# Optimization experiments

Measured on AMD Instinct MI355X. Metric: run time of the kernel, lower is better.

Reference implementation:

```python
import jax, jax.numpy as jnp
import numpy as np
from jax import lax

B, N, T, F, H, R = 32, 1024, 32, 5, 64, 5


def setup_inputs() -> dict:
    key = jax.random.key(0)
    ks = jax.random.split(key, 12)
    sc = 0.1
    x = jax.random.normal(ks[0], (B, N, T, F), dtype=jnp.float32)
    A = jax.random.randint(ks[1], (N, N, R), 0, 2).astype(jnp.float32)
    return {
        "x": x,
        "A": A,
        # nn.LSTM params (torch layout: [4H, in], gate order i,f,g,o)
        "lstm_Wih": jax.random.normal(ks[2], (4 * H, F), dtype=jnp.float32) * sc,
        "lstm_Whh": jax.random.normal(ks[3], (4 * H, H), dtype=jnp.float32) * sc,
        "lstm_bih": jax.random.normal(ks[4], (4 * H,), dtype=jnp.float32) * sc,
        "lstm_bhh": jax.random.normal(ks[5], (4 * H,), dtype=jnp.float32) * sc,
        # attention Linear(H, 1)
        "attn_w": jax.random.normal(ks[6], (1, H), dtype=jnp.float32) * sc,
        "attn_b": jax.random.normal(ks[7], (1,), dtype=jnp.float32) * sc,
        # GNN edge-gate Linear(R, 1)
        "gnn_w": jax.random.normal(ks[8], (1, R), dtype=jnp.float32) * sc,
        "gnn_b": jax.random.normal(ks[9], (1,), dtype=jnp.float32) * sc,
        # pred Linear(2H, 1)
        "pred_w": jax.random.normal(ks[10], (1, 2 * H), dtype=jnp.float32) * sc,
        "pred_b": jax.random.normal(ks[11], (1,), dtype=jnp.float32) * sc,
    }


def _lstm_attn(x, Wih, Whh, bih, bhh, attn_w, attn_b):
    # x: [BN, T, F] -> attended hidden [BN, H]
    BN, Tt, _ = x.shape
    Hh = Whh.shape[1]
    pre = x @ Wih.T + (bih + bhh)  # [BN, T, 4H] input projections precomputed

    def step(carry, xt):
        h, c = carry
        gates = xt + h @ Whh.T
        i, f, g, o = jnp.split(gates, 4, axis=-1)
        c = jax.nn.sigmoid(f) * c + jax.nn.sigmoid(i) * jnp.tanh(g)
        h = jax.nn.sigmoid(o) * jnp.tanh(c)
        return (h, c), h

    init = (jnp.zeros((BN, Hh), x.dtype), jnp.zeros((BN, Hh), x.dtype))
    _, hs = lax.scan(step, init, pre.transpose(1, 0, 2))
    hs = hs.transpose(1, 0, 2)  # [BN, T, H]
    scores = jnp.tanh(hs @ attn_w.T + attn_b)      # [BN, T, 1]
    aw = jax.nn.softmax(scores, axis=1)            # softmax over time
    return jnp.sum(hs * aw, axis=1)                # [BN, H]


def reference(x, A, lstm_Wih, lstm_Whh, lstm_bih, lstm_bhh,
              attn_w, attn_b, gnn_w, gnn_b, pred_w, pred_b):
    Bb, Nn, Tt, Ff = x.shape
    Hh = lstm_Whh.shape[1]
    # LSTM+attention shared across stocks -> fold stocks into batch
    e_old = _lstm_attn(x.reshape(Bb * Nn, Tt, Ff), lstm_Wih, lstm_Whh,
                       lstm_bih, lstm_bhh, attn_w, attn_b).reshape(Bb, Nn, Hh)

    # GNN: per-edge gate w[i,j] = LeakyReLU(Linear(A[i,j,:])), active if sum(A[i,j])>0
    mask = (jnp.sum(A, axis=-1) > 0).astype(e_old.dtype)             # [N, N]
    w = jax.nn.leaky_relu((A @ gnn_w.T + gnn_b)[..., 0], 0.2)        # [N, N]
    deg = jnp.sum(mask, axis=1)                                      # [N] active neighbor count
    coef = mask * w                                                  # [N, N]
    dots = jnp.einsum('bik,bjk->bij', e_old, e_old)                  # [B, N, N]
    e_new = jnp.einsum('bij,ij,bjk->bik', dots, coef, e_old) / deg[None, :, None]
    e_final = jnp.concatenate([e_old, e_new], axis=-1)               # [B, N, 2H]
    preds = e_final @ pred_w.T + pred_b                              # [B, N, 1]
    return preds
```

## Files before the change

kernel.cpp:

```cpp
#include <hip/hip_runtime.h>

constexpr int Bc = 32, Nc = 1024, Tc = 32, Fc = 5, Hc = 64;
constexpr int BNc = Bc * Nc;

#define DEVFN __device__ __forceinline__

typedef _Float16 f16x8 __attribute__((ext_vector_type(8)));
typedef _Float16 f16x4 __attribute__((ext_vector_type(4)));
typedef float    f32x16 __attribute__((ext_vector_type(16)));

DEVFN float fast_rcp(float x) { return __builtin_amdgcn_rcpf(x); }
DEVFN float tanh_fast(float x) { return 1.f - 2.f * fast_rcp(__expf(2.f * x) + 1.f); }

__global__ __launch_bounds__(128, 2) void lstm_attn_kernel(
    const float* __restrict__ x,
    const float* __restrict__ Wih,
    const float* __restrict__ Whh,
    const float* __restrict__ bih,
    const float* __restrict__ bhh,
    const float* __restrict__ attn_w,
    const float* __restrict__ attn_b,
    _Float16* __restrict__ E16,
    _Float16* __restrict__ ET)
{
    constexpr int XP = 164;
    __shared__ __align__(16) _Float16 xs[32 * XP];
    __shared__ __align__(16) _Float16 hb[2][32 * 64];
    __shared__ float ap[2][32];
    float* es = (float*)xs;

    const int tid  = threadIdx.x;
    const int w    = tid >> 6;
    const int lane = tid & 63;
    const int m    = lane & 31;
    const int hi   = lane >> 5;

    const float* xg = x + (size_t)blockIdx.x * 32 * Tc * Fc;
    for (int i = tid; i < 32 * 160; i += 128) {
        int mm = i / 160, o = i - mm * 160;
        xs[mm * XP + o] = (_Float16)xg[i];
    }
    for (int i = tid; i < 1024; i += 128) ((uint*)&hb[0][0])[i] = 0u;

    f16x8 af[4][5];
    #pragma unroll
    for (int g = 0; g < 4; ++g) {
        const int j = 32 * (2 * g + w) + m;
        #pragma unroll
        for (int kt = 0; kt < 4; ++kt) {
            const float* wp = Whh + j * 64 + kt * 16 + 8 * hi;
            float4 u0 = *(const float4*)wp;
            float4 u1 = *(const float4*)(wp + 4);
            af[g][kt] = f16x8{(_Float16)u0.x, (_Float16)u0.y, (_Float16)u0.z, (_Float16)u0.w,
                              (_Float16)u1.x, (_Float16)u1.y, (_Float16)u1.z, (_Float16)u1.w};
        }
        float v[8];
        #pragma unroll
        for (int e = 0; e < 5; ++e) v[e] = Wih[j * Fc + e];
        v[5] = bih[j] + bhh[j]; v[6] = 0.f; v[7] = 0.f;
        #pragma unroll
        for (int e = 0; e < 8; ++e) {
            float z = hi ? 0.f : v[e];
            af[g][4][e] = (_Float16)z;
        }
    }

    float aw_own[16];
    #pragma unroll
    for (int a2 = 0; a2 < 4; ++a2)
        #pragma unroll
        for (int p = 0; p < 4; ++p)
            aw_own[a2 * 4 + p] = attn_w[32 * w + 8 * a2 + 4 * hi + p];
    const float ab = attn_b[0];

    float hcur[16], cst[16], oacc[16];
    #pragma unroll
    for (int i = 0; i < 16; ++i) { hcur[i] = 0.f; cst[i] = 0.f; oacc[i] = 0.f; }
    float lsum = 0.f;

    f32x16 zero16 = {0,0,0,0,0,0,0,0,0,0,0,0,0,0,0,0};
    const int xrow = m * XP;
    const int swz  = m & 15;
    __syncthreads();

    f16x8 bf[5];
    #pragma unroll
    for (int kt = 0; kt < 4; ++kt) {
        f16x4 lo = *(const f16x4*)&hb[0][m * 64 + ((4 * kt + 2 * hi)     ^ swz) * 4];
        f16x4 hh = *(const f16x4*)&hb[0][m * 64 + ((4 * kt + 2 * hi + 1) ^ swz) * 4];
        bf[kt] = f16x8{lo[0], lo[1], lo[2], lo[3], hh[0], hh[1], hh[2], hh[3]};
    }
    {
        #pragma unroll
        for (int e = 0; e < 8; ++e) bf[4][e] = (_Float16)0.f;
        if (!hi) {
            #pragma unroll
            for (int e = 0; e < 5; ++e) bf[4][e] = xs[xrow + e];
            bf[4][5] = (_Float16)1.f;
        }
    }

    #pragma unroll 1
    for (int t = 0; t < Tc; ++t) {
        f32x16 acc[4];
        #pragma unroll
        for (int g = 0; g < 4; ++g) {
            acc[g] = __builtin_amdgcn_mfma_f32_32x32x16_f16(af[g][0], bf[0], zero16, 0, 0, 0);
            #pragma unroll
            for (int kt = 1; kt < 5; ++kt)
                acc[g] = __builtin_amdgcn_mfma_f32_32x32x16_f16(af[g][kt], bf[kt], acc[g], 0, 0, 0);
        }
        float attnp = 0.f;
        #pragma unroll
        for (int r = 0; r < 16; ++r) {
            float ei = __expf(-acc[0][r]);
            float ef = __expf(-acc[1][r]);
            float Eg = __expf(2.f * acc[2][r]);
            float eo = __expf(-acc[3][r]);
            float u  = 1.f + ei;
            float v  = 1.f + ef;
            float wq = Eg + 1.f;
            float z  = Eg - 1.f;
            float t1 = u * wq;
            float num = fmaf(cst[r], t1, z * v);
            float cn = num * fast_rcp(t1 * v);
            cst[r] = cn;
            float E2 = __expf(2.f * cn);
            float hv = (E2 - 1.f) * fast_rcp((E2 + 1.f) * (1.f + eo));
            hcur[r] = hv;
            attnp = fmaf(hv, aw_own[r], attnp);
        }
        _Float16* hw = &hb[(t + 1) & 1][0];
        #pragma unroll
        for (int a2 = 0; a2 < 4; ++a2) {
            f16x4 pk = {(_Float16)hcur[4 * a2 + 0], (_Float16)hcur[4 * a2 + 1],
                        (_Float16)hcur[4 * a2 + 2], (_Float16)hcur[4 * a2 + 3]};
            *(f16x4*)&hw[m * 64 + ((8 * w + 2 * a2 + hi) ^ swz) * 4] = pk;
        }
        attnp += __shfl_xor(attnp, 32);
        if (!hi) ap[w][m] = attnp;
        __syncthreads();
        float sc = tanh_fast(ap[0][m] + ap[1][m] + ab);
        float ew = __expf(sc);
        lsum += ew;
        #pragma unroll
        for (int i = 0; i < 16; ++i) oacc[i] = fmaf(ew, hcur[i], oacc[i]);
        if (t != Tc - 1) {
            const _Float16* hr = &hb[(t + 1) & 1][0];
            #pragma unroll
            for (int kt = 0; kt < 4; ++kt) {
                f16x4 lo = *(const f16x4*)&hr[m * 64 + ((4 * kt + 2 * hi)     ^ swz) * 4];
                f16x4 hh = *(const f16x4*)&hr[m * 64 + ((4 * kt + 2 * hi + 1) ^ swz) * 4];
                bf[kt] = f16x8{lo[0], lo[1], lo[2], lo[3], hh[0], hh[1], hh[2], hh[3]};
            }
            if (!hi) {
                #pragma unroll
                for (int e = 0; e < 5; ++e) bf[4][e] = xs[xrow + (t + 1) * Fc + e];
                bf[4][5] = (_Float16)1.f;
            }
        }
    }

    __syncthreads();
    const float li = fast_rcp(lsum);
    #pragma unroll
    for (int r = 0; r < 16; ++r) {
        int u = 32 * w + 8 * (r >> 2) + 4 * hi + (r & 3);
        es[m * 65 + u] = oacc[r] * li;
    }
    __syncthreads();

    uint* E16u = (uint*)E16 + (size_t)blockIdx.x * 32 * 32;
    for (int idx = tid; idx < 32 * 32; idx += 128) {
        int mm = idx >> 5, hp = idx & 31;
        union { _Float16 h2[2]; uint u; } cv;
        cv.h2[0] = (_Float16)es[mm * 65 + 2 * hp];
        cv.h2[1] = (_Float16)es[mm * 65 + 2 * hp + 1];
        E16u[idx] = cv.u;
    }
    const int bb_ = blockIdx.x >> 5, n0d = (blockIdx.x & 31) * 16;
    uint* ETu = (uint*)ET;
    for (int idx = tid; idx < 64 * 16; idx += 128) {
        int h = idx >> 4, c = idx & 15;
        union { _Float16 h2[2]; uint u; } cv;
        cv.h2[0] = (_Float16)es[(2 * c) * 65 + h];
        cv.h2[1] = (_Float16)es[(2 * c + 1) * 65 + h];
        ETu[((size_t)bb_ * 64 + h) * 512 + n0d + c] = cv.u;
    }
}

__global__ __launch_bounds__(256) void coefq_kernel(
    const float* __restrict__ A,
    const float* __restrict__ gnn_w,
    const float* __restrict__ gnn_b,
    float* __restrict__ coefQ,
    float* __restrict__ deg)
{
    __shared__ float ct[64 * 68];
    const int t = threadIdx.x;
    const int it = blockIdx.x >> 4, jt = blockIdx.x & 15;
    const int i_loc = t >> 2, chunk = t & 3;
    float gw[5];
    #pragma unroll
    for (int f = 0; f < 5; ++f) gw[f] = gnn_w[f];
    const float gb = gnn_b[0];

    const float* Ab = A + ((size_t)(it * 64 + i_loc) * 1024 + jt * 64 + chunk * 16) * 5;
    float buf[80];
    #pragma unroll
    for (int k = 0; k < 20; ++k)
        *(float4*)&buf[4 * k] = ((const float4*)Ab)[k];

    float cnt = 0.f;
    #pragma unroll
    for (int jj = 0; jj < 16; ++jj) {
        float s = 0.f, d = gb;
        #pragma unroll
        for (int f = 0; f < 5; ++f) { float vv = buf[5 * jj + f]; s += vv; d = fmaf(vv, gw[f], d); }
        float cf = (s > 0.f) ? (d >= 0.f ? d : 0.2f * d) : 0.f;
        ct[i_loc * 68 + chunk * 16 + jj] = cf;
        cnt += (s > 0.f) ? 1.f : 0.f;
    }
    cnt += __shfl_xor(cnt, 1);
    cnt += __shfl_xor(cnt, 2);
    if ((t & 3) == 0) atomicAdd(&deg[it * 64 + i_loc], cnt);
    __syncthreads();

    const int i_o = t & 63;
    #pragma unroll
    for (int p = 0; p < 4; ++p) {
        int jg = (t >> 6) + 4 * p;
        float4 v = *(const float4*)&ct[i_o * 68 + 4 * jg];
        ((float4*)coefQ)[(size_t)(jt * 16 + jg) * 1024 + it * 64 + i_o] = v;
    }
}

__global__ __launch_bounds__(256, 2) void gnn_pred_kernel(
    const _Float16* __restrict__ E16,
    const _Float16* __restrict__ ET,
    const float* __restrict__ coefQ,
    const float* __restrict__ deg,
    const float* __restrict__ pred_w,
    const float* __restrict__ pred_b,
    float* __restrict__ preds)
{
    __shared__ __align__(16) _Float16 tiles[2][4][64 * 64];
    const int tid  = threadIdx.x;
    const int w    = tid >> 6;
    const int lane = tid & 63;
    const int l31  = lane & 31;
    const int hi   = lane >> 5;
    const int b    = blockIdx.x >> 4;
    const int it   = blockIdx.x & 15;

    _Float16* EA = &tiles[0][w][0];
    _Float16* EB = &tiles[1][w][0];
    const float4* coefQ4 = (const float4*)coefQ;

    f16x8 eb[2][4];
    #pragma unroll
    for (int ni = 0; ni < 2; ++ni)
        #pragma unroll
        for (int kt = 0; kt < 4; ++kt)
            eb[ni][kt] = *(const f16x8*)(E16 +
                ((size_t)(b * 1024 + it * 64 + ni * 32 + l31) * 64 + 16 * kt + 8 * hi));

    f32x16 zero16 = {0,0,0,0,0,0,0,0,0,0,0,0,0,0,0,0};
    f32x16 oacc[2][2];
    #pragma unroll
    for (int mi = 0; mi < 2; ++mi)
        #pragma unroll
        for (int nh = 0; nh < 2; ++nh) oacc[mi][nh] = zero16;

    #pragma unroll 1
    for (int s = 0; s < 4; ++s) {
        const int jt = w * 4 + s;
        const _Float16* srcA = E16 + (size_t)(b * 1024 + jt * 64) * 64;
        const _Float16* srcB = ET + (size_t)b * 64 * 1024 + jt * 64;
        #pragma unroll
        for (int q = 0; q < 8; ++q) {
            int f = q * 64 + lane, r = f >> 3, c = f & 7;
            uint4 va = *(const uint4*)(srcA + r * 64 + c * 8);
            *(uint4*)(EA + r * 64 + ((c ^ (r & 7)) * 8)) = va;
            uint4 vb = *(const uint4*)(srcB + r * 1024 + c * 8);
            *(uint4*)(EB + r * 64 + ((c ^ (r & 7)) * 8)) = vb;
        }
        #pragma unroll 1
        for (int mj = 0; mj < 2; ++mj) {
            f16x8 af[4];
            #pragma unroll
            for (int kt = 0; kt < 4; ++kt)
                af[kt] = *(const f16x8*)(EA + (mj * 32 + l31) * 64 +
                                         (((2 * kt + hi) ^ (l31 & 7)) * 8));
            #pragma unroll
            for (int mi = 0; mi < 2; ++mi) {
                f32x16 a = __builtin_amdgcn_mfma_f32_32x32x16_f16(af[0], eb[mi][0], zero16, 0, 0, 0);
                #pragma unroll
                for (int kt = 1; kt < 4; ++kt)
                    a = __builtin_amdgcn_mfma_f32_32x32x16_f16(af[kt], eb[mi][kt], a, 0, 0, 0);
                #pragma unroll
                for (int rg = 0; rg < 4; ++rg) {
                    int j0 = jt * 64 + mj * 32 + 8 * rg + 4 * hi;
                    float4 cf = coefQ4[(size_t)(j0 >> 2) * 1024 + it * 64 + mi * 32 + l31];
                    a[4 * rg + 0] *= cf.x; a[4 * rg + 1] *= cf.y;
                    a[4 * rg + 2] *= cf.z; a[4 * rg + 3] *= cf.w;
                }
                f16x8 pa[2];
                #pragma unroll
                for (int kk = 0; kk < 2; ++kk) {
                    const int rg = 2 * kk;
                    #pragma unroll
                    for (int c4 = 0; c4 < 4; ++c4) {
                        float own_lo = a[rg * 4 + c4];
                        float own_hi = a[(rg + 1) * 4 + c4];
                        float send = hi ? own_lo : own_hi;
                        float recv = __shfl_xor(send, 32);
                        float lo = hi ? recv : own_lo;
                        float hv = hi ? own_hi : recv;
                        pa[kk][c4]     = (_Float16)lo;
                        pa[kk][4 + c4] = (_Float16)hv;
                    }
                }
                #pragma unroll
                for (int nh = 0; nh < 2; ++nh)
                    #pragma unroll
                    for (int kk = 0; kk < 2; ++kk) {
                        const int ktj = 2 * mj + kk;
                        f16x8 bb = *(const f16x8*)(EB + (nh * 32 + l31) * 64 +
                                                   (((2 * ktj + hi) ^ (l31 & 7)) * 8));
                        oacc[mi][nh] = __builtin_amdgcn_mfma_f32_32x32x16_f16(
                            pa[kk], bb, oacc[mi][nh], 0, 0, 0);
                    }
            }
        }
    }

    const float pwh0 = pred_w[64 + l31];
    const float pwh1 = pred_w[96 + l31];
    #pragma unroll
    for (int mi = 0; mi < 2; ++mi)
        #pragma unroll
        for (int r = 0; r < 16; ++r) {
            float v = oacc[mi][0][r] * pwh0 + oacc[mi][1][r] * pwh1;
            v += __shfl_xor(v, 1);  v += __shfl_xor(v, 2);  v += __shfl_xor(v, 4);
            v += __shfl_xor(v, 8);  v += __shfl_xor(v, 16);
            int i_loc = mi * 32 + 8 * (r >> 2) + (r & 3) + 4 * hi;
            int gi = it * 64 + i_loc;
            if (l31 == 0) {
                float dg = deg[gi];
                atomicAdd(&preds[b * 1024 + gi], v * fast_rcp(dg));
            }
        }
    if (w == 0) {
        const float pb0 = pred_b[0];
        #pragma unroll
        for (int ni = 0; ni < 2; ++ni) {
            float dot = 0.f;
            #pragma unroll
            for (int kt = 0; kt < 4; ++kt)
                #pragma unroll
                for (int e = 0; e < 8; ++e)
                    dot = fmaf((float)eb[ni][kt][e], pred_w[16 * kt + 8 * hi + e], dot);
            dot += __shfl_xor(dot, 32);
            if (hi == 0)
                atomicAdd(&preds[b * 1024 + it * 64 + ni * 32 + l31], dot + pb0);
        }
    }
}

extern "C" void kernel_launch(void* const* d_in, const int* in_sizes, int n_in,
                              void* d_out, int out_size, void* d_ws, size_t ws_size,
                              hipStream_t stream) {
    const float* x      = (const float*)d_in[0];
    const float* A      = (const float*)d_in[1];
    const float* Wih    = (const float*)d_in[2];
    const float* Whh    = (const float*)d_in[3];
    const float* bih    = (const float*)d_in[4];
    const float* bhh    = (const float*)d_in[5];
    const float* attn_w = (const float*)d_in[6];
    const float* attn_b = (const float*)d_in[7];
    const float* gnn_w  = (const float*)d_in[8];
    const float* gnn_b  = (const float*)d_in[9];
    const float* pred_w = (const float*)d_in[10];
    const float* pred_b = (const float*)d_in[11];
    float* preds = (float*)d_out;

    _Float16* E16 = (_Float16*)d_ws;
    _Float16* ET  = E16 + (size_t)BNc * Hc;
    float* coefQ  = (float*)(ET + (size_t)BNc * Hc);
    float* deg    = coefQ + (size_t)Nc * Nc;

    hipMemsetAsync(preds, 0, (size_t)out_size * sizeof(float), stream);
    hipMemsetAsync(deg, 0, Nc * sizeof(float), stream);

    lstm_attn_kernel<<<BNc / 32, 128, 0, stream>>>(x, Wih, Whh, bih, bhh,
                                                   attn_w, attn_b, E16, ET);
    coefq_kernel<<<256, 256, 0, stream>>>(A, gnn_w, gnn_b, coefQ, deg);
    gnn_pred_kernel<<<Bc * (Nc / 64), 256, 0, stream>>>(E16, ET, coefQ, deg,
                                                        pred_w, pred_b, preds);
}
```

Baseline: 239.7 us.

## Remove atomics and memsets via per-tile degree partials and shared-memory reduction

The coef kernel is retiled to 32x32 blocks with coalesced staging of A through shared memory, and it writes per-column-tile degree partials instead of atomically accumulating degrees. The GNN/pred kernel reduces the four waves' partial outputs in shared memory, sums the degree partials itself and writes predictions directly, so both memsets and all global atomics go away. Block order is also swapped so that consecutive blocks share the same row tile. The cost is 32 extra degree loads per output and an added block barrier.

```diff
diff --git a/kernel.cpp b/kernel.cpp
--- a/kernel.cpp
+++ b/kernel.cpp
@@ -189,57 +189,59 @@
     }
 }
 
-__global__ __launch_bounds__(256) void coefq_kernel(
+__global__ __launch_bounds__(256, 4) void coefq_kernel(
     const float* __restrict__ A,
     const float* __restrict__ gnn_w,
     const float* __restrict__ gnn_b,
     float* __restrict__ coefQ,
-    float* __restrict__ deg)
+    float* __restrict__ degP)
 {
-    __shared__ float ct[64 * 68];
-    const int t = threadIdx.x;
-    const int it = blockIdx.x >> 4, jt = blockIdx.x & 15;
-    const int i_loc = t >> 2, chunk = t & 3;
+    constexpr int CP = 162;
+    __shared__ float as[32 * CP];
+    __shared__ float dcnt[4][32];
+    const int t  = threadIdx.x;
+    const int it = blockIdx.x >> 5, jt = blockIdx.x & 31;
+
     float gw[5];
     #pragma unroll
     for (int f = 0; f < 5; ++f) gw[f] = gnn_w[f];
     const float gb = gnn_b[0];
 
-    const float* Ab = A + ((size_t)(it * 64 + i_loc) * 1024 + jt * 64 + chunk * 16) * 5;
-    float buf[80];
-    #pragma unroll
-    for (int k = 0; k < 20; ++k)
-        *(float4*)&buf[4 * k] = ((const float4*)Ab)[k];
-
-    float cnt = 0.f;
-    #pragma unroll
-    for (int jj = 0; jj < 16; ++jj) {
+    const float* src = A + ((size_t)it * 32 * 1024 + jt * 32) * 5;
+    #pragma unroll
+    for (int k = 0; k < 10; ++k) {
+        int idx = t + k * 256;
+        int row = idx / 80, c2 = idx - row * 80;
+        *(float2*)&as[row * CP + c2 * 2] = *(const float2*)(src + (size_t)row * 5120 + c2 * 2);
+    }
+    __syncthreads();
+
+    const int g = t >> 5, i_loc = t & 31;
+    float cf[4]; float cnt = 0.f;
+    #pragma unroll
+    for (int q = 0; q < 4; ++q) {
+        const float* ap = &as[i_loc * CP + (g * 4 + q) * 5];
         float s = 0.f, d = gb;
         #pragma unroll
-        for (int f = 0; f < 5; ++f) { float vv = buf[5 * jj + f]; s += vv; d = fmaf(vv, gw[f], d); }
-        float cf = (s > 0.f) ? (d >= 0.f ? d : 0.2f * d) : 0.f;
-        ct[i_loc * 68 + chunk * 16 + jj] = cf;
+        for (int f = 0; f < 5; ++f) { float vv = ap[f]; s += vv; d = fmaf(vv, gw[f], d); }
+        cf[q] = (s > 0.f) ? (d >= 0.f ? d : 0.2f * d) : 0.f;
         cnt += (s > 0.f) ? 1.f : 0.f;
     }
-    cnt += __shfl_xor(cnt, 1);
-    cnt += __shfl_xor(cnt, 2);
-    if ((t & 3) == 0) atomicAdd(&deg[it * 64 + i_loc], cnt);
-    __syncthreads();
-
-    const int i_o = t & 63;
-    #pragma unroll
-    for (int p = 0; p < 4; ++p) {
-        int jg = (t >> 6) + 4 * p;
-        float4 v = *(const float4*)&ct[i_o * 68 + 4 * jg];
-        ((float4*)coefQ)[(size_t)(jt * 16 + jg) * 1024 + it * 64 + i_o] = v;
-    }
+    ((float4*)coefQ)[(size_t)(jt * 8 + g) * 1024 + it * 32 + i_loc] =
+        float4{cf[0], cf[1], cf[2], cf[3]};
+
+    cnt += __shfl_xor(cnt, 32);
+    if ((t & 32) == 0) dcnt[t >> 6][i_loc] = cnt;
+    __syncthreads();
+    if (t < 32)
+        degP[jt * 1024 + it * 32 + t] = dcnt[0][t] + dcnt[1][t] + dcnt[2][t] + dcnt[3][t];
 }
 
 __global__ __launch_bounds__(256, 2) void gnn_pred_kernel(
     const _Float16* __restrict__ E16,
     const _Float16* __restrict__ ET,
     const float* __restrict__ coefQ,
-    const float* __restrict__ deg,
+    const float* __restrict__ degP,
     const float* __restrict__ pred_w,
     const float* __restrict__ pred_b,
     float* __restrict__ preds)
@@ -250,8 +252,8 @@
     const int lane = tid & 63;
     const int l31  = lane & 31;
     const int hi   = lane >> 5;
-    const int b    = blockIdx.x >> 4;
-    const int it   = blockIdx.x & 15;
+    const int it   = blockIdx.x >> 5;
+    const int b    = blockIdx.x & 31;
 
     _Float16* EA = &tiles[0][w][0];
     _Float16* EB = &tiles[1][w][0];
@@ -335,6 +337,7 @@
         }
     }
 
+    float* pacc = (float*)&tiles[0][w][0];
     const float pwh0 = pred_w[64 + l31];
     const float pwh1 = pred_w[96 + l31];
     #pragma unroll
@@ -345,12 +348,9 @@
             v += __shfl_xor(v, 1);  v += __shfl_xor(v, 2);  v += __shfl_xor(v, 4);
             v += __shfl_xor(v, 8);  v += __shfl_xor(v, 16);
             int i_loc = mi * 32 + 8 * (r >> 2) + (r & 3) + 4 * hi;
-            int gi = it * 64 + i_loc;
-            if (l31 == 0) {
-                float dg = deg[gi];
-                atomicAdd(&preds[b * 1024 + gi], v * fast_rcp(dg));
-            }
-        }
+            if (l31 == 0) pacc[i_loc] = v;
+        }
+    __syncthreads();
     if (w == 0) {
         const float pb0 = pred_b[0];
         #pragma unroll
@@ -362,8 +362,18 @@
                 for (int e = 0; e < 8; ++e)
                     dot = fmaf((float)eb[ni][kt][e], pred_w[16 * kt + 8 * hi + e], dot);
             dot += __shfl_xor(dot, 32);
-            if (hi == 0)
-                atomicAdd(&preds[b * 1024 + it * 64 + ni * 32 + l31], dot + pb0);
+            if (hi == 0) {
+                int i_loc = ni * 32 + l31;
+                int gi = it * 64 + i_loc;
+                float osum = ((float*)&tiles[0][0][0])[i_loc] +
+                             ((float*)&tiles[0][1][0])[i_loc] +
+                             ((float*)&tiles[0][2][0])[i_loc] +
+                             ((float*)&tiles[0][3][0])[i_loc];
+                float dsum = 0.f;
+                #pragma unroll
+                for (int jj = 0; jj < 32; ++jj) dsum += degP[jj * 1024 + gi];
+                preds[b * 1024 + gi] = dot + osum * fast_rcp(dsum) + pb0;
+            }
         }
     }
 }
@@ -388,14 +398,11 @@
     _Float16* E16 = (_Float16*)d_ws;
     _Float16* ET  = E16 + (size_t)BNc * Hc;
     float* coefQ  = (float*)(ET + (size_t)BNc * Hc);
-    float* deg    = coefQ + (size_t)Nc * Nc;
-
-    hipMemsetAsync(preds, 0, (size_t)out_size * sizeof(float), stream);
-    hipMemsetAsync(deg, 0, Nc * sizeof(float), stream);
+    float* degP   = coefQ + (size_t)Nc * Nc;
 
     lstm_attn_kernel<<<BNc / 32, 128, 0, stream>>>(x, Wih, Whh, bih, bhh,
                                                    attn_w, attn_b, E16, ET);
-    coefq_kernel<<<256, 256, 0, stream>>>(A, gnn_w, gnn_b, coefQ, deg);
-    gnn_pred_kernel<<<Bc * (Nc / 64), 256, 0, stream>>>(E16, ET, coefQ, deg,
+    coefq_kernel<<<1024, 256, 0, stream>>>(A, gnn_w, gnn_b, coefQ, degP);
+    gnn_pred_kernel<<<Bc * (Nc / 64), 256, 0, stream>>>(E16, ET, coefQ, degP,
                                                         pred_w, pred_b, preds);
 }
```

After: 223.6 us. -6.7%, faster.
